# Performance work log

Measured on AMD Instinct MI355X. Metric: run time of the kernel, lower is better.

## Reference

```python
import jax, jax.numpy as jnp
import numpy as np

H = 128
NUM_LAYERS = 3
IN_DIM = 32


def setup_inputs() -> dict:
    key = jax.random.key(0)
    ks = jax.random.split(key, 16)
    B, L = 2, 512
    coords = jax.random.normal(ks[0], (B, L, 3), dtype=jnp.float32) * 10.0
    contacts = (jax.random.uniform(ks[1], (B, L, L)) < 0.1).astype(jnp.float32)
    node_feats = jax.random.normal(ks[2], (B, L, IN_DIM), dtype=jnp.float32)
    s = lambda fan_in: 1.0 / np.sqrt(fan_in)
    in_w = jax.random.normal(ks[3], (IN_DIM, H), dtype=jnp.float32) * s(IN_DIM)
    in_b = jnp.zeros((H,), dtype=jnp.float32)
    # per-layer stacked params
    e_w1 = jax.random.normal(ks[4], (NUM_LAYERS, 2 * H + 2, H), dtype=jnp.float32) * s(2 * H + 2)
    e_b1 = jnp.zeros((NUM_LAYERS, H), dtype=jnp.float32)
    e_w2 = jax.random.normal(ks[5], (NUM_LAYERS, H, H), dtype=jnp.float32) * s(H)
    e_b2 = jnp.zeros((NUM_LAYERS, H), dtype=jnp.float32)
    n_w1 = jax.random.normal(ks[6], (NUM_LAYERS, 2 * H, H), dtype=jnp.float32) * s(2 * H)
    n_b1 = jnp.zeros((NUM_LAYERS, H), dtype=jnp.float32)
    n_w2 = jax.random.normal(ks[7], (NUM_LAYERS, H, H), dtype=jnp.float32) * s(H)
    n_b2 = jnp.zeros((NUM_LAYERS, H), dtype=jnp.float32)
    return dict(coords=coords, contacts=contacts, node_feats=node_feats,
                in_w=in_w, in_b=in_b,
                e_w1=e_w1, e_b1=e_b1, e_w2=e_w2, e_b2=e_b2,
                n_w1=n_w1, n_b1=n_b1, n_w2=n_w2, n_b2=n_b2)


def _forward(coords, contacts, node_feats, in_w, in_b,
             e_w1, e_b1, e_w2, e_b2, n_w1, n_b1, n_w2, n_b2):
    # input projection
    h = node_feats @ in_w + in_b  # (B,L,H)
    # pairwise distances (safe norm: grad 0 on the zero diagonal)
    diff = coords[:, :, None, :] - coords[:, None, :, :]  # (B,L,L,3)
    sq = jnp.sum(diff * diff, axis=-1, keepdims=True)      # (B,L,L,1)
    dist = jnp.where(sq > 0, jnp.sqrt(jnp.where(sq > 0, sq, 1.0)), 0.0)
    contact_ij = contacts[..., None]                        # (B,L,L,1)
    edge_mask = (contacts > 0)[..., None]                   # (B,L,L,1)
    for layer in range(NUM_LAYERS):
        w1 = e_w1[layer]
        # split the first edge-linear over the concat [hi, hj, dist, contact]
        hi_part = h @ w1[:H]              # (B,L,H) -> broadcast over j
        hj_part = h @ w1[H:2 * H]         # (B,L,H) -> broadcast over i
        pre = (hi_part[:, :, None, :] + hj_part[:, None, :, :]
               + dist * w1[2 * H] + contact_ij * w1[2 * H + 1] + e_b1[layer])
        m_ij = jax.nn.silu(jax.nn.silu(pre) @ e_w2[layer] + e_b2[layer])  # (B,L,L,H)
        m_i = jnp.sum(jnp.where(edge_mask, m_ij, 0.0), axis=2)            # (B,L,H)
        # node MLP on concat([h, m_i]) via split linear
        w1n = n_w1[layer]
        npre = h @ w1n[:H] + m_i @ w1n[H:] + n_b1[layer]
        delta_h = jax.nn.silu(npre) @ n_w2[layer] + n_b2[layer]
        h = h + delta_h
    return h


def reference(coords, contacts, node_feats, in_w, in_b,
              e_w1, e_b1, e_w2, e_b2, n_w1, n_b1, n_w2, n_b2):
    return _forward(coords, contacts, node_feats, in_w, in_b,
                    e_w1, e_b1, e_w2, e_b2, n_w1, n_b1, n_w2, n_b2)
```

## Files before the change

### kernel.cpp

```cpp
#include <hip/hip_runtime.h>
#include <hip/hip_bf16.h>


#define Hc 128
#define Lc 512
#define ROWS 1024

typedef __bf16 bf16x8 __attribute__((ext_vector_type(8)));
typedef float  f32x4  __attribute__((ext_vector_type(4)));

__device__ __forceinline__ float silu(float x) {
    return x / (1.f + __expf(-x));
}

__global__ __launch_bounds__(256) void prep_all(
    const float* __restrict__ contacts,
    unsigned short* __restrict__ elist, int* __restrict__ ecnt,
    const float* __restrict__ in_w, const float* __restrict__ e_w1,
    const float* __restrict__ e_w2, const float* __restrict__ n_w1,
    const float* __restrict__ n_w2,
    __bf16* __restrict__ in_wt, __bf16* __restrict__ w1et,
    __bf16* __restrict__ w2te, __bf16* __restrict__ w1nt,
    __bf16* __restrict__ w2nt) {
    int blk = blockIdx.x;
    if (blk < 256) {
        int r = blk * 4 + (threadIdx.x >> 6);
        int lane = threadIdx.x & 63;
        const float* row = contacts + (size_t)r * Lc;
        int cnt = 0;
        for (int base = 0; base < Lc; base += 64) {
            float v = row[base + lane];
            unsigned long long mask = __ballot(v > 0.f);
            if (v > 0.f) {
                int pos = cnt + __popcll(mask & ((1ull << lane) - 1ull));
                elist[r * Lc + pos] = (unsigned short)(base + lane);
            }
            cnt += __popcll(mask);
        }
        if (lane == 0) ecnt[r] = cnt;
        return;
    }
    int idx = (blk - 256) * 256 + threadIdx.x;
    if (idx < 4096) {
        int col = idx >> 5, k = idx & 31;
        in_wt[idx] = (__bf16)in_w[k * Hc + col];
    } else if (idx < 4096 + 98304) {
        int q = idx - 4096;
        int l = q / 32768, r = q % 32768;
        int col = r >> 7, k = r & 127;
        float v = (col < 128) ? e_w1[(size_t)l * 258 * Hc + k * Hc + col]
                              : e_w1[(size_t)l * 258 * Hc + (128 + k) * Hc + (col - 128)];
        w1et[q] = (__bf16)v;
    } else if (idx < 4096 + 98304 + 49152) {
        int q = idx - 4096 - 98304;
        int l = q / 16384, r = q % 16384;
        int col = r >> 7, k = r & 127;
        w2te[q] = (__bf16)e_w2[(size_t)l * 16384 + k * Hc + col];
    } else if (idx < 4096 + 98304 + 49152 + 98304) {
        int q = idx - 4096 - 98304 - 49152;
        int l = q / 32768, r = q % 32768;
        int col = r >> 8, k = r & 255;
        w1nt[q] = (__bf16)n_w1[(size_t)l * 32768 + k * Hc + col];
    } else {
        int q = idx - 4096 - 98304 - 49152 - 98304;
        int l = q / 16384, r = q % 16384;
        int col = r >> 7, k = r & 127;
        w2nt[q] = (__bf16)n_w2[(size_t)l * 16384 + k * Hc + col];
    }
}

__global__ __launch_bounds__(256) void input_mfma(
    const float* __restrict__ nf, const __bf16* __restrict__ in_wt,
    const float* __restrict__ in_b,
    const __bf16* __restrict__ w1et0, const float* __restrict__ b1e,
    const float* __restrict__ fold,
    float* __restrict__ h, float* __restrict__ hi, float* __restrict__ hj) {
    int r0 = blockIdx.x * 16;
    int t = threadIdx.x;
    int l = t & 63, w = t >> 6;
    int lr = l & 15, g = l >> 4;
    __shared__ __bf16 A0[16 * 32];
    __shared__ __bf16 A3[16 * Hc];

    if (t < 64) {
        int row = t >> 2, blk = t & 3, k0 = blk * 8;
        const float* src = &nf[(size_t)(r0 + row) * 32 + k0];
        float4 v0 = *(const float4*)src, v1 = *(const float4*)(src + 4);
        bf16x8 o;
        o[0] = (__bf16)v0.x; o[1] = (__bf16)v0.y; o[2] = (__bf16)v0.z; o[3] = (__bf16)v0.w;
        o[4] = (__bf16)v1.x; o[5] = (__bf16)v1.y; o[6] = (__bf16)v1.z; o[7] = (__bf16)v1.w;
        *(bf16x8*)&A0[row * 32 + (blk ^ (row & 3)) * 8] = o;
    }
    int c0 = w * 32;
    bf16x8 bf0[2];
#pragma unroll
    for (int nt = 0; nt < 2; nt++)
        bf0[nt] = *(const bf16x8*)&in_wt[(size_t)(c0 + nt * 16 + lr) * 32 + g * 8];
    __syncthreads();
    f32x4 acc[2] = {};
    {
        bf16x8 a = *(const bf16x8*)&A0[lr * 32 + (g ^ (lr & 3)) * 8];
        acc[0] = __builtin_amdgcn_mfma_f32_16x16x32_bf16(a, bf0[0], acc[0], 0, 0, 0);
        acc[1] = __builtin_amdgcn_mfma_f32_16x16x32_bf16(a, bf0[1], acc[1], 0, 0, 0);
    }
#pragma unroll
    for (int nt = 0; nt < 2; nt++) {
        int col = c0 + nt * 16 + lr;
        float bb = in_b[col];
#pragma unroll
        for (int j = 0; j < 4; j++) {
            int row = g * 4 + j;
            float hv = acc[nt][j] + bb;
            h[(size_t)(r0 + row) * Hc + col] = hv;
            A3[row * Hc + ((col >> 3) ^ (row & 7)) * 8 + (col & 7)] = (__bf16)hv;
        }
    }
    __syncthreads();
    int c3 = w * 64;
    bf16x8 b3[4][4];
#pragma unroll
    for (int nt = 0; nt < 4; nt++)
#pragma unroll
        for (int ks = 0; ks < 4; ks++)
            b3[nt][ks] = *(const bf16x8*)&w1et0[
                (size_t)(c3 + nt * 16 + lr) * Hc + ks * 32 + g * 8];
    f32x4 acc3[4] = {};
#pragma unroll
    for (int ks = 0; ks < 4; ks++) {
        bf16x8 a = *(const bf16x8*)&A3[lr * Hc + (((ks * 4 + g) ^ (lr & 7))) * 8];
#pragma unroll
        for (int nt = 0; nt < 4; nt++)
            acc3[nt] = __builtin_amdgcn_mfma_f32_16x16x32_bf16(a, b3[nt][ks], acc3[nt], 0, 0, 0);
    }
#pragma unroll
    for (int nt = 0; nt < 4; nt++) {
        int col = c3 + nt * 16 + lr;
#pragma unroll
        for (int j = 0; j < 4; j++) {
            int row = g * 4 + j;
            if (col < 128)
                hi[(size_t)(r0 + row) * Hc + col] = acc3[nt][j] + b1e[col] + fold[col];
            else
                hj[(size_t)(r0 + row) * Hc + (col - 128)] = acc3[nt][j];
        }
    }
}

__global__ __launch_bounds__(256) void edge_kernel(
    const float* __restrict__ hi, const float* __restrict__ hj,
    const float* __restrict__ coords,
    const unsigned short* __restrict__ elist, const int* __restrict__ ecnt,
    const float* __restrict__ w1d, const __bf16* __restrict__ w2t,
    const float* __restrict__ b2, float* __restrict__ m_part) {
    int r = blockIdx.x >> 1, half = blockIdx.x & 1;
    int b = r >> 9;
    int i = r & (Lc - 1);
    int t = threadIdx.x;
    int l = t & 63, w = t >> 6;
    int lr = l & 15, g = l >> 4;

    __shared__ __bf16 S[32 * Hc];

    float* mp = m_part + ((size_t)half * ROWS + r) * Hc;
    int cnt = ecnt[r];

    bf16x8 bf[2][4];
#pragma unroll
    for (int nt = 0; nt < 2; nt++)
#pragma unroll
        for (int kk = 0; kk < 4; kk++)
            bf[nt][kk] = *(const bf16x8*)&w2t[
                (size_t)(w * 32 + nt * 16 + lr) * Hc + kk * 32 + g * 8];
    float b2v[2] = { b2[w * 32 + lr], b2[w * 32 + 16 + lr] };
    float msum[2] = { 0.f, 0.f };

    int e_f = t >> 3;
    int cg  = t & 7;
    int c0  = cg * 16;
    float cxi = coords[(b * Lc + i) * 3 + 0];
    float cyi = coords[(b * Lc + i) * 3 + 1];
    float czi = coords[(b * Lc + i) * 3 + 2];
    float4 hi4[4], wd4[4];
#pragma unroll
    for (int q = 0; q < 4; q++) {
        hi4[q] = *(const float4*)&hi[(size_t)r * Hc + c0 + q * 4];
        wd4[q] = *(const float4*)&w1d[c0 + q * 4];
    }
    const float* hjb = hj + (size_t)(b * Lc) * Hc;

    int first = half * 32;
    for (int base = first; base < cnt; base += 64) {
        if (base != first) __syncthreads();
        int nloc = cnt - base; if (nloc > 32) nloc = 32;
        bf16x8 o0, o1;
        if (e_f < nloc) {
            int j = elist[r * Lc + base + e_f];
            float dx = cxi - coords[(b * Lc + j) * 3 + 0];
            float dy = cyi - coords[(b * Lc + j) * 3 + 1];
            float dz = czi - coords[(b * Lc + j) * 3 + 2];
            float d = sqrtf(dx * dx + dy * dy + dz * dz);
            const float* hjrow = hjb + (size_t)j * Hc + c0;
            float v[16];
#pragma unroll
            for (int q = 0; q < 4; q++) {
                float4 hjv = *(const float4*)&hjrow[q * 4];
                v[q * 4 + 0] = silu(hi4[q].x + hjv.x + d * wd4[q].x);
                v[q * 4 + 1] = silu(hi4[q].y + hjv.y + d * wd4[q].y);
                v[q * 4 + 2] = silu(hi4[q].z + hjv.z + d * wd4[q].z);
                v[q * 4 + 3] = silu(hi4[q].w + hjv.w + d * wd4[q].w);
            }
#pragma unroll
            for (int u = 0; u < 8; u++) {
                o0[u] = (__bf16)v[u];
                o1[u] = (__bf16)v[8 + u];
            }
        } else {
#pragma unroll
            for (int u = 0; u < 8; u++) { o0[u] = (__bf16)0.f; o1[u] = (__bf16)0.f; }
        }
        int sw = e_f & 7;
        *(bf16x8*)&S[e_f * Hc + ((cg * 2) ^ sw) * 8]     = o0;
        *(bf16x8*)&S[e_f * Hc + ((cg * 2 + 1) ^ sw) * 8] = o1;
        __syncthreads();

        f32x4 acc[2][2] = {};
#pragma unroll
        for (int ks = 0; ks < 4; ks++) {
            bf16x8 a0 = *(const bf16x8*)&S[lr * Hc + ((ks * 4 + g) ^ (lr & 7)) * 8];
            bf16x8 a1 = *(const bf16x8*)&S[(16 + lr) * Hc + ((ks * 4 + g) ^ (lr & 7)) * 8];
            acc[0][0] = __builtin_amdgcn_mfma_f32_16x16x32_bf16(a0, bf[0][ks], acc[0][0], 0, 0, 0);
            acc[0][1] = __builtin_amdgcn_mfma_f32_16x16x32_bf16(a0, bf[1][ks], acc[0][1], 0, 0, 0);
            acc[1][0] = __builtin_amdgcn_mfma_f32_16x16x32_bf16(a1, bf[0][ks], acc[1][0], 0, 0, 0);
            acc[1][1] = __builtin_amdgcn_mfma_f32_16x16x32_bf16(a1, bf[1][ks], acc[1][1], 0, 0, 0);
        }

#pragma unroll
        for (int mt = 0; mt < 2; mt++)
#pragma unroll
            for (int nt = 0; nt < 2; nt++)
#pragma unroll
                for (int jj = 0; jj < 4; jj++) {
                    if (mt * 16 + g * 4 + jj < nloc)
                        msum[nt] += silu(acc[mt][nt][jj] + b2v[nt]);
                }
    }

    float v0 = msum[0]; v0 += __shfl_xor(v0, 16); v0 += __shfl_xor(v0, 32);
    float v1 = msum[1]; v1 += __shfl_xor(v1, 16); v1 += __shfl_xor(v1, 32);
    if (l < 16) {
        mp[w * 32 + l]      = v0;
        mp[w * 32 + 16 + l] = v1;
    }
}

__global__ __launch_bounds__(256) void node_mfma(
    const float* __restrict__ h, const float* __restrict__ m0,
    const float* __restrict__ m1,
    const __bf16* __restrict__ w1nt, const float* __restrict__ b1n,
    const __bf16* __restrict__ w2nt, const float* __restrict__ b2n,
    float* __restrict__ hout, int do_hij,
    const __bf16* __restrict__ w1et, const float* __restrict__ b1e,
    const float* __restrict__ fold,
    float* __restrict__ hi, float* __restrict__ hj) {
    int r0 = blockIdx.x * 16;
    int t = threadIdx.x;
    int l = t & 63, w = t >> 6;
    int lr = l & 15, g = l >> 4;
    __shared__ __bf16 A1[16 * 256];
    __shared__ __bf16 A2[16 * Hc];
    __shared__ __bf16 A3[16 * Hc];
    __shared__ float hbuf[16 * Hc];

#pragma unroll
    for (int it = 0; it < 2; it++) {
        int idx = t + it * 256;
        int row = idx >> 5, blk = idx & 31, k0 = blk * 8;
        float4 v0, v1;
        if (k0 < 128) {
            const float* src = &h[(size_t)(r0 + row) * Hc + k0];
            v0 = *(const float4*)src; v1 = *(const float4*)(src + 4);
            *(float4*)&hbuf[row * Hc + k0] = v0;
            *(float4*)&hbuf[row * Hc + k0 + 4] = v1;
        } else {
            const float* s0 = &m0[(size_t)(r0 + row) * Hc + (k0 - 128)];
            const float* s1 = &m1[(size_t)(r0 + row) * Hc + (k0 - 128)];
            float4 a0 = *(const float4*)s0, a1 = *(const float4*)(s0 + 4);
            float4 c0v = *(const float4*)s1, c1 = *(const float4*)(s1 + 4);
            v0.x = a0.x + c0v.x; v0.y = a0.y + c0v.y;
            v0.z = a0.z + c0v.z; v0.w = a0.w + c0v.w;
            v1.x = a1.x + c1.x; v1.y = a1.y + c1.y;
            v1.z = a1.z + c1.z; v1.w = a1.w + c1.w;
        }
        bf16x8 o;
        o[0] = (__bf16)v0.x; o[1] = (__bf16)v0.y; o[2] = (__bf16)v0.z; o[3] = (__bf16)v0.w;
        o[4] = (__bf16)v1.x; o[5] = (__bf16)v1.y; o[6] = (__bf16)v1.z; o[7] = (__bf16)v1.w;
        *(bf16x8*)&A1[row * 256 + (blk ^ (row & 7)) * 8] = o;
    }
    int c0 = w * 32;
    bf16x8 b1f[2][8];
#pragma unroll
    for (int nt = 0; nt < 2; nt++)
#pragma unroll
        for (int ks = 0; ks < 8; ks++)
            b1f[nt][ks] = *(const bf16x8*)&w1nt[
                (size_t)(c0 + nt * 16 + lr) * 256 + ks * 32 + g * 8];
    __syncthreads();

    f32x4 acc[2] = {};
#pragma unroll
    for (int ks = 0; ks < 8; ks++) {
        bf16x8 a = *(const bf16x8*)&A1[lr * 256 + (((ks * 4 + g) ^ (lr & 7))) * 8];
        acc[0] = __builtin_amdgcn_mfma_f32_16x16x32_bf16(a, b1f[0][ks], acc[0], 0, 0, 0);
        acc[1] = __builtin_amdgcn_mfma_f32_16x16x32_bf16(a, b1f[1][ks], acc[1], 0, 0, 0);
    }
#pragma unroll
    for (int nt = 0; nt < 2; nt++) {
        int col = c0 + nt * 16 + lr;
        float bb = b1n[col];
#pragma unroll
        for (int j = 0; j < 4; j++) {
            int row = g * 4 + j;
            A2[row * Hc + ((col >> 3) ^ (row & 7)) * 8 + (col & 7)] =
                (__bf16)silu(acc[nt][j] + bb);
        }
    }
    __syncthreads();

    bf16x8 b2f[2][4];
#pragma unroll
    for (int nt = 0; nt < 2; nt++)
#pragma unroll
        for (int ks = 0; ks < 4; ks++)
            b2f[nt][ks] = *(const bf16x8*)&w2nt[
                (size_t)(c0 + nt * 16 + lr) * Hc + ks * 32 + g * 8];
    f32x4 acc2[2] = {};
#pragma unroll
    for (int ks = 0; ks < 4; ks++) {
        bf16x8 a = *(const bf16x8*)&A2[lr * Hc + (((ks * 4 + g) ^ (lr & 7))) * 8];
        acc2[0] = __builtin_amdgcn_mfma_f32_16x16x32_bf16(a, b2f[0][ks], acc2[0], 0, 0, 0);
        acc2[1] = __builtin_amdgcn_mfma_f32_16x16x32_bf16(a, b2f[1][ks], acc2[1], 0, 0, 0);
    }
#pragma unroll
    for (int nt = 0; nt < 2; nt++) {
        int col = c0 + nt * 16 + lr;
        float bb = b2n[col];
#pragma unroll
        for (int j = 0; j < 4; j++) {
            int row = g * 4 + j;
            float hnew = hbuf[row * Hc + col] + acc2[nt][j] + bb;
            hout[(size_t)(r0 + row) * Hc + col] = hnew;
            A3[row * Hc + ((col >> 3) ^ (row & 7)) * 8 + (col & 7)] = (__bf16)hnew;
        }
    }
    if (!do_hij) return;
    __syncthreads();

    int c3 = w * 64;
    bf16x8 b3[4][4];
#pragma unroll
    for (int nt = 0; nt < 4; nt++)
#pragma unroll
        for (int ks = 0; ks < 4; ks++)
            b3[nt][ks] = *(const bf16x8*)&w1et[
                (size_t)(c3 + nt * 16 + lr) * Hc + ks * 32 + g * 8];
    f32x4 acc3[4] = {};
#pragma unroll
    for (int ks = 0; ks < 4; ks++) {
        bf16x8 a = *(const bf16x8*)&A3[lr * Hc + (((ks * 4 + g) ^ (lr & 7))) * 8];
#pragma unroll
        for (int nt = 0; nt < 4; nt++)
            acc3[nt] = __builtin_amdgcn_mfma_f32_16x16x32_bf16(a, b3[nt][ks], acc3[nt], 0, 0, 0);
    }
#pragma unroll
    for (int nt = 0; nt < 4; nt++) {
        int col = c3 + nt * 16 + lr;
#pragma unroll
        for (int j = 0; j < 4; j++) {
            int row = g * 4 + j;
            if (col < 128)
                hi[(size_t)(r0 + row) * Hc + col] = acc3[nt][j] + b1e[col] + fold[col];
            else
                hj[(size_t)(r0 + row) * Hc + (col - 128)] = acc3[nt][j];
        }
    }
}

extern "C" void kernel_launch(void* const* d_in, const int* in_sizes, int n_in,
                              void* d_out, int out_size, void* d_ws, size_t ws_size,
                              hipStream_t stream) {
    const float* coords     = (const float*)d_in[0];
    const float* contacts   = (const float*)d_in[1];
    const float* node_feats = (const float*)d_in[2];
    const float* in_w       = (const float*)d_in[3];
    const float* in_b       = (const float*)d_in[4];
    const float* e_w1       = (const float*)d_in[5];
    const float* e_b1       = (const float*)d_in[6];
    const float* e_w2       = (const float*)d_in[7];
    const float* e_b2       = (const float*)d_in[8];
    const float* n_w1       = (const float*)d_in[9];
    const float* n_b1       = (const float*)d_in[10];
    const float* n_w2       = (const float*)d_in[11];
    const float* n_b2       = (const float*)d_in[12];

    float* ws = (float*)d_ws;
    float* h  = ws;
    float* hi = ws + 131072;
    float* hj = ws + 262144;
    unsigned short* elist = (unsigned short*)(ws + 524288);
    int*   ecnt = (int*)(ws + 786432);
    __bf16* in_wt = (__bf16*)(ws + 787456);
    __bf16* w1et  = (__bf16*)(ws + 789504);
    __bf16* w2te  = (__bf16*)(ws + 838656);
    __bf16* w1nt  = (__bf16*)(ws + 863232);
    __bf16* w2nt  = (__bf16*)(ws + 912384);
    float* m_part = ws + 936960;
    float* m0 = m_part;
    float* m1 = m_part + 131072;

    prep_all<<<256 + 1168, 256, 0, stream>>>(
        contacts, elist, ecnt,
        in_w, e_w1, e_w2, n_w1, n_w2,
        in_wt, w1et, w2te, w1nt, w2nt);
    input_mfma<<<ROWS / 16, 256, 0, stream>>>(
        node_feats, in_wt, in_b,
        w1et, e_b1, e_w1 + (size_t)257 * Hc,
        h, hi, hj);

    for (int l = 0; l < 3; l++) {
        const float* w1 = e_w1 + (size_t)l * 258 * Hc;
        edge_kernel<<<ROWS * 2, 256, 0, stream>>>(hi, hj, coords, elist, ecnt,
                                                  w1 + 2 * Hc * Hc,
                                                  w2te + (size_t)l * Hc * Hc,
                                                  e_b2 + l * Hc, m_part);
        int do_hij = (l < 2);
        int lnext = (l + 1 < 3) ? l + 1 : 0;
        float* hout = (l == 2) ? (float*)d_out : h;
        node_mfma<<<ROWS / 16, 256, 0, stream>>>(
            h, m0, m1,
            w1nt + (size_t)l * 128 * 256, n_b1 + l * Hc,
            w2nt + (size_t)l * 128 * 128, n_b2 + l * Hc,
            hout, do_hij,
            w1et + (size_t)lnext * 256 * 128, e_b1 + lnext * Hc,
            e_w1 + (size_t)lnext * 258 * Hc + (size_t)257 * Hc,
            hi, hj);
    }
}
```

Baseline: 184.6 us.

## Remove prep kernel: build edge lists in-block and load weights directly from fp32

Drops the prep_all kernel. Each edge block now compacts its own contact row into a shared-memory j-list, and the MFMA kernels gather and convert weight fragments straight from the original fp32 weights with strided loads instead of reading pre-transposed bf16 copies. The edge kernel also goes from two half-blocks per row to one block per row, so the partial-sum buffers and their addition in node_mfma go away. This removes one launch and the workspace round trips, at the cost of strided uncoalesced weight loads in every block and half as many edge blocks, which means less parallelism and longer serial edge loops per block.

```diff
diff --git a/kernel.cpp b/kernel.cpp
--- a/kernel.cpp
+++ b/kernel.cpp
@@ -13,67 +13,18 @@
     return x / (1.f + __expf(-x));
 }
 
-__global__ __launch_bounds__(256) void prep_all(
-    const float* __restrict__ contacts,
-    unsigned short* __restrict__ elist, int* __restrict__ ecnt,
-    const float* __restrict__ in_w, const float* __restrict__ e_w1,
-    const float* __restrict__ e_w2, const float* __restrict__ n_w1,
-    const float* __restrict__ n_w2,
-    __bf16* __restrict__ in_wt, __bf16* __restrict__ w1et,
-    __bf16* __restrict__ w2te, __bf16* __restrict__ w1nt,
-    __bf16* __restrict__ w2nt) {
-    int blk = blockIdx.x;
-    if (blk < 256) {
-        int r = blk * 4 + (threadIdx.x >> 6);
-        int lane = threadIdx.x & 63;
-        const float* row = contacts + (size_t)r * Lc;
-        int cnt = 0;
-        for (int base = 0; base < Lc; base += 64) {
-            float v = row[base + lane];
-            unsigned long long mask = __ballot(v > 0.f);
-            if (v > 0.f) {
-                int pos = cnt + __popcll(mask & ((1ull << lane) - 1ull));
-                elist[r * Lc + pos] = (unsigned short)(base + lane);
-            }
-            cnt += __popcll(mask);
-        }
-        if (lane == 0) ecnt[r] = cnt;
-        return;
-    }
-    int idx = (blk - 256) * 256 + threadIdx.x;
-    if (idx < 4096) {
-        int col = idx >> 5, k = idx & 31;
-        in_wt[idx] = (__bf16)in_w[k * Hc + col];
-    } else if (idx < 4096 + 98304) {
-        int q = idx - 4096;
-        int l = q / 32768, r = q % 32768;
-        int col = r >> 7, k = r & 127;
-        float v = (col < 128) ? e_w1[(size_t)l * 258 * Hc + k * Hc + col]
-                              : e_w1[(size_t)l * 258 * Hc + (128 + k) * Hc + (col - 128)];
-        w1et[q] = (__bf16)v;
-    } else if (idx < 4096 + 98304 + 49152) {
-        int q = idx - 4096 - 98304;
-        int l = q / 16384, r = q % 16384;
-        int col = r >> 7, k = r & 127;
-        w2te[q] = (__bf16)e_w2[(size_t)l * 16384 + k * Hc + col];
-    } else if (idx < 4096 + 98304 + 49152 + 98304) {
-        int q = idx - 4096 - 98304 - 49152;
-        int l = q / 32768, r = q % 32768;
-        int col = r >> 8, k = r & 255;
-        w1nt[q] = (__bf16)n_w1[(size_t)l * 32768 + k * Hc + col];
-    } else {
-        int q = idx - 4096 - 98304 - 49152 - 98304;
-        int l = q / 16384, r = q % 16384;
-        int col = r >> 7, k = r & 127;
-        w2nt[q] = (__bf16)n_w2[(size_t)l * 16384 + k * Hc + col];
-    }
+__device__ __forceinline__ bf16x8 load_fragT(const float* __restrict__ W,
+                                             int col, int k0, int ldw) {
+    bf16x8 o;
+#pragma unroll
+    for (int u = 0; u < 8; u++) o[u] = (__bf16)W[(size_t)(k0 + u) * ldw + col];
+    return o;
 }
 
 __global__ __launch_bounds__(256) void input_mfma(
-    const float* __restrict__ nf, const __bf16* __restrict__ in_wt,
+    const float* __restrict__ nf, const float* __restrict__ in_w,
     const float* __restrict__ in_b,
-    const __bf16* __restrict__ w1et0, const float* __restrict__ b1e,
-    const float* __restrict__ fold,
+    const float* __restrict__ e_w1_0, const float* __restrict__ b1e,
     float* __restrict__ h, float* __restrict__ hi, float* __restrict__ hj) {
     int r0 = blockIdx.x * 16;
     int t = threadIdx.x;
@@ -95,7 +46,7 @@
     bf16x8 bf0[2];
 #pragma unroll
     for (int nt = 0; nt < 2; nt++)
-        bf0[nt] = *(const bf16x8*)&in_wt[(size_t)(c0 + nt * 16 + lr) * 32 + g * 8];
+        bf0[nt] = load_fragT(in_w, c0 + nt * 16 + lr, g * 8, Hc);
     __syncthreads();
     f32x4 acc[2] = {};
     {
@@ -119,11 +70,20 @@
     int c3 = w * 64;
     bf16x8 b3[4][4];
 #pragma unroll
-    for (int nt = 0; nt < 4; nt++)
-#pragma unroll
-        for (int ks = 0; ks < 4; ks++)
-            b3[nt][ks] = *(const bf16x8*)&w1et0[
-                (size_t)(c3 + nt * 16 + lr) * Hc + ks * 32 + g * 8];
+    for (int nt = 0; nt < 4; nt++) {
+        int col = c3 + nt * 16 + lr;
+        const float* Wb = (col < 128) ? (e_w1_0 + col)
+                                      : (e_w1_0 + 128 * Hc + (col - 128));
+#pragma unroll
+        for (int ks = 0; ks < 4; ks++) {
+            int k0 = ks * 32 + g * 8;
+            bf16x8 o;
+#pragma unroll
+            for (int u = 0; u < 8; u++) o[u] = (__bf16)Wb[(size_t)(k0 + u) * Hc];
+            b3[nt][ks] = o;
+        }
+    }
+    const float* fold = e_w1_0 + (size_t)257 * Hc;
     f32x4 acc3[4] = {};
 #pragma unroll
     for (int ks = 0; ks < 4; ks++) {
@@ -148,11 +108,10 @@
 
 __global__ __launch_bounds__(256) void edge_kernel(
     const float* __restrict__ hi, const float* __restrict__ hj,
-    const float* __restrict__ coords,
-    const unsigned short* __restrict__ elist, const int* __restrict__ ecnt,
-    const float* __restrict__ w1d, const __bf16* __restrict__ w2t,
-    const float* __restrict__ b2, float* __restrict__ m_part) {
-    int r = blockIdx.x >> 1, half = blockIdx.x & 1;
+    const float* __restrict__ coords, const float* __restrict__ contacts,
+    const float* __restrict__ w1d, const float* __restrict__ e_w2_l,
+    const float* __restrict__ b2, float* __restrict__ m_out) {
+    int r = blockIdx.x;
     int b = r >> 9;
     int i = r & (Lc - 1);
     int t = threadIdx.x;
@@ -160,17 +119,30 @@
     int lr = l & 15, g = l >> 4;
 
     __shared__ __bf16 S[32 * Hc];
-
-    float* mp = m_part + ((size_t)half * ROWS + r) * Hc;
-    int cnt = ecnt[r];
+    __shared__ unsigned short jlist[Lc];
+    __shared__ int cnt_s;
+
+    if (t < 64) {
+        const float* crow = contacts + (size_t)r * Lc;
+        int c = 0;
+        for (int seg = 0; seg < Lc; seg += 64) {
+            float v = crow[seg + t];
+            unsigned long long mask = __ballot(v > 0.f);
+            if (v > 0.f) {
+                int pos = c + __popcll(mask & ((1ull << t) - 1ull));
+                jlist[pos] = (unsigned short)(seg + t);
+            }
+            c += __popcll(mask);
+        }
+        if (t == 0) cnt_s = c;
+    }
 
     bf16x8 bf[2][4];
 #pragma unroll
     for (int nt = 0; nt < 2; nt++)
 #pragma unroll
         for (int kk = 0; kk < 4; kk++)
-            bf[nt][kk] = *(const bf16x8*)&w2t[
-                (size_t)(w * 32 + nt * 16 + lr) * Hc + kk * 32 + g * 8];
+            bf[nt][kk] = load_fragT(e_w2_l, w * 32 + nt * 16 + lr, kk * 32 + g * 8, Hc);
     float b2v[2] = { b2[w * 32 + lr], b2[w * 32 + 16 + lr] };
     float msum[2] = { 0.f, 0.f };
 
@@ -188,13 +160,15 @@
     }
     const float* hjb = hj + (size_t)(b * Lc) * Hc;
 
-    int first = half * 32;
-    for (int base = first; base < cnt; base += 64) {
-        if (base != first) __syncthreads();
+    __syncthreads();
+    int cnt = cnt_s;
+
+    for (int base = 0; base < cnt; base += 32) {
+        if (base) __syncthreads();
         int nloc = cnt - base; if (nloc > 32) nloc = 32;
         bf16x8 o0, o1;
         if (e_f < nloc) {
-            int j = elist[r * Lc + base + e_f];
+            int j = jlist[base + e_f];
             float dx = cxi - coords[(b * Lc + j) * 3 + 0];
             float dy = cyi - coords[(b * Lc + j) * 3 + 1];
             float dz = czi - coords[(b * Lc + j) * 3 + 2];
@@ -248,19 +222,17 @@
     float v0 = msum[0]; v0 += __shfl_xor(v0, 16); v0 += __shfl_xor(v0, 32);
     float v1 = msum[1]; v1 += __shfl_xor(v1, 16); v1 += __shfl_xor(v1, 32);
     if (l < 16) {
-        mp[w * 32 + l]      = v0;
-        mp[w * 32 + 16 + l] = v1;
+        m_out[(size_t)r * Hc + w * 32 + l]      = v0;
+        m_out[(size_t)r * Hc + w * 32 + 16 + l] = v1;
     }
 }
 
 __global__ __launch_bounds__(256) void node_mfma(
-    const float* __restrict__ h, const float* __restrict__ m0,
-    const float* __restrict__ m1,
-    const __bf16* __restrict__ w1nt, const float* __restrict__ b1n,
-    const __bf16* __restrict__ w2nt, const float* __restrict__ b2n,
+    const float* __restrict__ h, const float* __restrict__ m,
+    const float* __restrict__ n_w1_l, const float* __restrict__ b1n,
+    const float* __restrict__ n_w2_l, const float* __restrict__ b2n,
     float* __restrict__ hout, int do_hij,
-    const __bf16* __restrict__ w1et, const float* __restrict__ b1e,
-    const float* __restrict__ fold,
+    const float* __restrict__ e_w1_n, const float* __restrict__ b1e,
     float* __restrict__ hi, float* __restrict__ hj) {
     int r0 = blockIdx.x * 16;
     int t = threadIdx.x;
@@ -275,26 +247,18 @@
     for (int it = 0; it < 2; it++) {
         int idx = t + it * 256;
         int row = idx >> 5, blk = idx & 31, k0 = blk * 8;
-        float4 v0, v1;
-        if (k0 < 128) {
-            const float* src = &h[(size_t)(r0 + row) * Hc + k0];
-            v0 = *(const float4*)src; v1 = *(const float4*)(src + 4);
-            *(float4*)&hbuf[row * Hc + k0] = v0;
-            *(float4*)&hbuf[row * Hc + k0 + 4] = v1;
-        } else {
-            const float* s0 = &m0[(size_t)(r0 + row) * Hc + (k0 - 128)];
-            const float* s1 = &m1[(size_t)(r0 + row) * Hc + (k0 - 128)];
-            float4 a0 = *(const float4*)s0, a1 = *(const float4*)(s0 + 4);
-            float4 c0v = *(const float4*)s1, c1 = *(const float4*)(s1 + 4);
-            v0.x = a0.x + c0v.x; v0.y = a0.y + c0v.y;
-            v0.z = a0.z + c0v.z; v0.w = a0.w + c0v.w;
-            v1.x = a1.x + c1.x; v1.y = a1.y + c1.y;
-            v1.z = a1.z + c1.z; v1.w = a1.w + c1.w;
-        }
+        const float* src = (k0 < 128)
+            ? &h[(size_t)(r0 + row) * Hc + k0]
+            : &m[(size_t)(r0 + row) * Hc + (k0 - 128)];
+        float4 v0 = *(const float4*)src, v1 = *(const float4*)(src + 4);
         bf16x8 o;
         o[0] = (__bf16)v0.x; o[1] = (__bf16)v0.y; o[2] = (__bf16)v0.z; o[3] = (__bf16)v0.w;
         o[4] = (__bf16)v1.x; o[5] = (__bf16)v1.y; o[6] = (__bf16)v1.z; o[7] = (__bf16)v1.w;
         *(bf16x8*)&A1[row * 256 + (blk ^ (row & 7)) * 8] = o;
+        if (k0 < 128) {
+            *(float4*)&hbuf[row * Hc + k0] = v0;
+            *(float4*)&hbuf[row * Hc + k0 + 4] = v1;
+        }
     }
     int c0 = w * 32;
     bf16x8 b1f[2][8];
@@ -302,8 +266,7 @@
     for (int nt = 0; nt < 2; nt++)
 #pragma unroll
         for (int ks = 0; ks < 8; ks++)
-            b1f[nt][ks] = *(const bf16x8*)&w1nt[
-                (size_t)(c0 + nt * 16 + lr) * 256 + ks * 32 + g * 8];
+            b1f[nt][ks] = load_fragT(n_w1_l, c0 + nt * 16 + lr, ks * 32 + g * 8, Hc);
     __syncthreads();
 
     f32x4 acc[2] = {};
@@ -331,8 +294,7 @@
     for (int nt = 0; nt < 2; nt++)
 #pragma unroll
         for (int ks = 0; ks < 4; ks++)
-            b2f[nt][ks] = *(const bf16x8*)&w2nt[
-                (size_t)(c0 + nt * 16 + lr) * Hc + ks * 32 + g * 8];
+            b2f[nt][ks] = load_fragT(n_w2_l, c0 + nt * 16 + lr, ks * 32 + g * 8, Hc);
     f32x4 acc2[2] = {};
 #pragma unroll
     for (int ks = 0; ks < 4; ks++) {
@@ -358,11 +320,20 @@
     int c3 = w * 64;
     bf16x8 b3[4][4];
 #pragma unroll
-    for (int nt = 0; nt < 4; nt++)
-#pragma unroll
-        for (int ks = 0; ks < 4; ks++)
-            b3[nt][ks] = *(const bf16x8*)&w1et[
-                (size_t)(c3 + nt * 16 + lr) * Hc + ks * 32 + g * 8];
+    for (int nt = 0; nt < 4; nt++) {
+        int col = c3 + nt * 16 + lr;
+        const float* Wb = (col < 128) ? (e_w1_n + col)
+                                      : (e_w1_n + 128 * Hc + (col - 128));
+#pragma unroll
+        for (int ks = 0; ks < 4; ks++) {
+            int k0 = ks * 32 + g * 8;
+            bf16x8 o;
+#pragma unroll
+            for (int u = 0; u < 8; u++) o[u] = (__bf16)Wb[(size_t)(k0 + u) * Hc];
+            b3[nt][ks] = o;
+        }
+    }
+    const float* fold = e_w1_n + (size_t)257 * Hc;
     f32x4 acc3[4] = {};
 #pragma unroll
     for (int ks = 0; ks < 4; ks++) {
@@ -406,42 +377,27 @@
     float* h  = ws;
     float* hi = ws + 131072;
     float* hj = ws + 262144;
-    unsigned short* elist = (unsigned short*)(ws + 524288);
-    int*   ecnt = (int*)(ws + 786432);
-    __bf16* in_wt = (__bf16*)(ws + 787456);
-    __bf16* w1et  = (__bf16*)(ws + 789504);
-    __bf16* w2te  = (__bf16*)(ws + 838656);
-    __bf16* w1nt  = (__bf16*)(ws + 863232);
-    __bf16* w2nt  = (__bf16*)(ws + 912384);
-    float* m_part = ws + 936960;
-    float* m0 = m_part;
-    float* m1 = m_part + 131072;
-
-    prep_all<<<256 + 1168, 256, 0, stream>>>(
-        contacts, elist, ecnt,
-        in_w, e_w1, e_w2, n_w1, n_w2,
-        in_wt, w1et, w2te, w1nt, w2nt);
+    float* m  = ws + 393216;
+
     input_mfma<<<ROWS / 16, 256, 0, stream>>>(
-        node_feats, in_wt, in_b,
-        w1et, e_b1, e_w1 + (size_t)257 * Hc,
-        h, hi, hj);
+        node_feats, in_w, in_b, e_w1, e_b1, h, hi, hj);
 
     for (int l = 0; l < 3; l++) {
         const float* w1 = e_w1 + (size_t)l * 258 * Hc;
-        edge_kernel<<<ROWS * 2, 256, 0, stream>>>(hi, hj, coords, elist, ecnt,
-                                                  w1 + 2 * Hc * Hc,
-                                                  w2te + (size_t)l * Hc * Hc,
-                                                  e_b2 + l * Hc, m_part);
+        edge_kernel<<<ROWS, 256, 0, stream>>>(
+            hi, hj, coords, contacts,
+            w1 + 2 * Hc * Hc,
+            e_w2 + (size_t)l * Hc * Hc,
+            e_b2 + l * Hc, m);
         int do_hij = (l < 2);
         int lnext = (l + 1 < 3) ? l + 1 : 0;
         float* hout = (l == 2) ? (float*)d_out : h;
         node_mfma<<<ROWS / 16, 256, 0, stream>>>(
-            h, m0, m1,
-            w1nt + (size_t)l * 128 * 256, n_b1 + l * Hc,
-            w2nt + (size_t)l * 128 * 128, n_b2 + l * Hc,
+            h, m,
+            n_w1 + (size_t)l * 256 * Hc, n_b1 + l * Hc,
+            n_w2 + (size_t)l * Hc * Hc,  n_b2 + l * Hc,
             hout, do_hij,
-            w1et + (size_t)lnext * 256 * 128, e_b1 + lnext * Hc,
-            e_w1 + (size_t)lnext * 258 * Hc + (size_t)257 * Hc,
+            e_w1 + (size_t)lnext * 258 * Hc, e_b1 + lnext * Hc,
             hi, hj);
     }
 }
```

Measured after the change: 181.9 us. About the same (-1.5%).
